# Kernel tuning notes

Measured on AMD Instinct MI355X. Metric: run time of the kernel, lower is better.

Reference implementation:

```python
import jax, jax.numpy as jnp
import numpy as np

N, E, D = 40000, 640000, 128
BN_EPS = 1e-5


def setup_inputs() -> dict:
    key = jax.random.key(0)
    ks = jax.random.split(key, 6)
    x = jax.random.normal(ks[0], (N, D), dtype=jnp.float32)
    src = jax.random.randint(ks[1], (E,), 0, N, dtype=jnp.int64)
    dst = jax.random.randint(ks[2], (E,), 0, N, dtype=jnp.int64)
    W1 = jax.random.normal(ks[3], (D, D), dtype=jnp.float32) * (1.0 / np.sqrt(D))
    b1 = jnp.zeros((D,), dtype=jnp.float32)
    gamma = jnp.ones((D,), dtype=jnp.float32)
    beta = jnp.zeros((D,), dtype=jnp.float32)
    W2 = jax.random.normal(ks[4], (D, D), dtype=jnp.float32) * (1.0 / np.sqrt(D))
    b2 = jnp.zeros((D,), dtype=jnp.float32)
    eps = jnp.zeros((1,), dtype=jnp.float32)
    return {"x": x, "src": src, "dst": dst, "W1": W1, "b1": b1,
            "gamma": gamma, "beta": beta, "W2": W2, "b2": b2, "eps": eps}


def reference(x, src, dst, W1, b1, gamma, beta, W2, b2, eps):
    # edge gather + ReLU + scatter-sum aggregation  (copy_u -> relu -> sum)
    m = jax.nn.relu(x[src])                                  # [E, D]
    agg = jax.ops.segment_sum(m, dst, num_segments=N)        # [N, D]
    h = (1.0 + eps[0]) * x + agg                             # eps-scaled residual
    # MLP: Linear -> BatchNorm1d (batch stats) -> ReLU -> Linear
    h = h @ W1.T + b1
    mu = jnp.mean(h, axis=0)
    var = jnp.var(h, axis=0)                                 # biased, as torch BN
    h = (h - mu) * jax.lax.rsqrt(var + BN_EPS) * gamma + beta
    h = jax.nn.relu(h)
    return h @ W2.T + b2
```

## Files before the change

kernel.cpp:

```cpp
#include <hip/hip_runtime.h>

#define NN 40000
#define NE 640000
#define DD 128
#define CAP 64

typedef __attribute__((ext_vector_type(8))) short short8;
typedef __attribute__((ext_vector_type(4))) float floatx4;

__device__ __forceinline__ unsigned short f2bf(float f) {
    union { float f; unsigned u; } v; v.f = f;
    return (unsigned short)((v.u + 0x7fffu + ((v.u >> 16) & 1u)) >> 16);
}
__device__ __forceinline__ float bflo2f(unsigned u) {
    union { unsigned u; float f; } v; v.u = u << 16; return v.f;
}
__device__ __forceinline__ float bfhi2f(unsigned u) {
    union { unsigned u; float f; } v; v.u = u & 0xffff0000u; return v.f;
}


__global__ void k_convert(const float* __restrict__ x, const float* __restrict__ W1,
                          const float* __restrict__ W2, unsigned short* __restrict__ xb,
                          unsigned short* __restrict__ W1b, unsigned short* __restrict__ W2b) {
    const int tid = blockIdx.x * 256 + threadIdx.x;
    const int P = gridDim.x * 256;
    const float4* x4 = (const float4*)x;
    for (int i = tid; i < NN * DD / 4; i += P) {
        float4 v = x4[i];
        ushort4 o;
        o.x = f2bf(v.x); o.y = f2bf(v.y); o.z = f2bf(v.z); o.w = f2bf(v.w);
        ((ushort4*)xb)[i] = o;
    }
    if (tid < 8192) {
        const float4* w4 = (tid < 4096) ? (const float4*)W1 : (const float4*)W2;
        unsigned short* wb = (tid < 4096) ? W1b : W2b;
        int i = tid & 4095;
        float4 v = w4[i];
        ushort4 o;
        o.x = f2bf(v.x); o.y = f2bf(v.y); o.z = f2bf(v.z); o.w = f2bf(v.w);
        ((ushort4*)wb)[i] = o;
    }
}

__global__ void k_bucket(const int* __restrict__ src, const int* __restrict__ dst,
                         int* __restrict__ cnt, unsigned short* __restrict__ eidx) {
    const int e = blockIdx.x * 256 + threadIdx.x;
    const int d = dst[e];
    const int s = src[e];
    const int slot = atomicAdd(&cnt[d], 1);
    if (slot < CAP) eidx[d * CAP + slot] = (unsigned short)s;
}

__launch_bounds__(256)
__global__ void k_gather(const unsigned short* __restrict__ xb,
                         const unsigned short* __restrict__ eidx,
                         const int* __restrict__ cnt, const float* __restrict__ eps,
                         unsigned short* __restrict__ h) {
    const int n = blockIdx.x * 4 + (threadIdx.x >> 6);
    const int lane = threadIdx.x & 63;
    const unsigned* xw = (const unsigned*)xb;
    const float s = 1.0f + eps[0];
    unsigned xv = xw[n * 64 + lane];
    float ax = bflo2f(xv) * s, ay = bfhi2f(xv) * s;
    int deg = cnt[n];
    deg = (deg > CAP) ? CAP : deg;
    const unsigned short* row = eidx + n * CAP;
    int j = 0;
    for (; j + 3 < deg; j += 4) {
        ushort4 s4 = *(const ushort4*)(row + j);
        unsigned v0 = xw[(int)s4.x * 64 + lane];
        unsigned v1 = xw[(int)s4.y * 64 + lane];
        unsigned v2 = xw[(int)s4.z * 64 + lane];
        unsigned v3 = xw[(int)s4.w * 64 + lane];
        ax += (fmaxf(bflo2f(v0), 0.f) + fmaxf(bflo2f(v1), 0.f)) +
              (fmaxf(bflo2f(v2), 0.f) + fmaxf(bflo2f(v3), 0.f));
        ay += (fmaxf(bfhi2f(v0), 0.f) + fmaxf(bfhi2f(v1), 0.f)) +
              (fmaxf(bfhi2f(v2), 0.f) + fmaxf(bfhi2f(v3), 0.f));
    }
    for (; j < deg; ++j) {
        unsigned v = xw[(int)row[j] * 64 + lane];
        ax += fmaxf(bflo2f(v), 0.f);
        ay += fmaxf(bfhi2f(v), 0.f);
    }
    ((unsigned*)h)[n * 64 + lane] = ((unsigned)f2bf(ay) << 16) | (unsigned)f2bf(ax);
}

__launch_bounds__(256)
__global__ void k_gemm1(const unsigned short* __restrict__ h,
                        const unsigned short* __restrict__ W1b,
                        const float* __restrict__ b1,
                        float* __restrict__ h1, float* __restrict__ stats) {
    __shared__ float red[2][4][DD];
    const int t = threadIdx.x;
    const int wv = t >> 6, lane = t & 63, m = lane & 15, q = lane >> 4;
    const int r0 = blockIdx.x * 64 + wv * 16;
    floatx4 acc[8];
    #pragma unroll
    for (int nt = 0; nt < 8; ++nt) acc[nt] = (floatx4){0.f, 0.f, 0.f, 0.f};
    const unsigned short* arow = h + (r0 + m) * DD + q * 8;
    const unsigned short* brow = W1b + m * DD + q * 8;
    #pragma unroll
    for (int kt = 0; kt < 4; ++kt) {
        short8 a = *(const short8*)(arow + kt * 32);
        #pragma unroll
        for (int nt = 0; nt < 8; ++nt) {
            short8 b = *(const short8*)(brow + nt * 16 * DD + kt * 32);
            acc[nt] = __builtin_amdgcn_mfma_f32_16x16x32_bf16(a, b, acc[nt], 0, 0, 0);
        }
    }
    #pragma unroll
    for (int nt = 0; nt < 8; ++nt) {
        float bv = b1[nt * 16 + m];
        float cs = 0.f, cq = 0.f;
        #pragma unroll
        for (int r = 0; r < 4; ++r) {
            float v = acc[nt][r] + bv;
            h1[(r0 + q * 4 + r) * DD + nt * 16 + m] = v;
            cs += v;
            cq = fmaf(v, v, cq);
        }
        cs += __shfl_xor(cs, 16); cs += __shfl_xor(cs, 32);
        cq += __shfl_xor(cq, 16); cq += __shfl_xor(cq, 32);
        if (q == 0) { red[0][wv][nt * 16 + m] = cs; red[1][wv][nt * 16 + m] = cq; }
    }
    __syncthreads();
    {
        int plane = t >> 7, j = t & 127;
        float v = (red[plane][0][j] + red[plane][1][j]) + (red[plane][2][j] + red[plane][3][j]);
        atomicAdd(stats + plane * DD + j, v);
    }
}

__launch_bounds__(256)
__global__ void k_gemm2(float* __restrict__ io, const unsigned short* __restrict__ W2b,
                        const float* __restrict__ b2, const float* __restrict__ stats,
                        const float* __restrict__ gamma, const float* __restrict__ beta) {
    __shared__ float ssc[DD], ssh[DD];
    const int t = threadIdx.x;
    if (t < DD) {
        const float inv_n = 1.0f / (float)NN;
        float mu = stats[t] * inv_n;
        float var = stats[DD + t] * inv_n - mu * mu;
        float sc = rsqrtf(var + 1e-5f) * gamma[t];
        ssc[t] = sc;
        ssh[t] = beta[t] - mu * sc;
    }
    __syncthreads();
    const int wv = t >> 6, lane = t & 63, m = lane & 15, q = lane >> 4;
    const int r0 = blockIdx.x * 64 + wv * 16;
    floatx4 acc[8];
    #pragma unroll
    for (int nt = 0; nt < 8; ++nt) acc[nt] = (floatx4){0.f, 0.f, 0.f, 0.f};
    const float* arow = io + (r0 + m) * DD + q * 8;
    const unsigned short* brow = W2b + m * DD + q * 8;
    #pragma unroll
    for (int kt = 0; kt < 4; ++kt) {
        const float* ap = arow + kt * 32;
        const int k0 = kt * 32 + q * 8;
        float4 v0 = *(const float4*)(ap);
        float4 v1 = *(const float4*)(ap + 4);
        float4 c0 = *(const float4*)(ssc + k0);
        float4 c1 = *(const float4*)(ssc + k0 + 4);
        float4 d0 = *(const float4*)(ssh + k0);
        float4 d1 = *(const float4*)(ssh + k0 + 4);
        short8 a;
        a[0] = (short)f2bf(fmaxf(fmaf(v0.x, c0.x, d0.x), 0.f));
        a[1] = (short)f2bf(fmaxf(fmaf(v0.y, c0.y, d0.y), 0.f));
        a[2] = (short)f2bf(fmaxf(fmaf(v0.z, c0.z, d0.z), 0.f));
        a[3] = (short)f2bf(fmaxf(fmaf(v0.w, c0.w, d0.w), 0.f));
        a[4] = (short)f2bf(fmaxf(fmaf(v1.x, c1.x, d1.x), 0.f));
        a[5] = (short)f2bf(fmaxf(fmaf(v1.y, c1.y, d1.y), 0.f));
        a[6] = (short)f2bf(fmaxf(fmaf(v1.z, c1.z, d1.z), 0.f));
        a[7] = (short)f2bf(fmaxf(fmaf(v1.w, c1.w, d1.w), 0.f));
        #pragma unroll
        for (int nt = 0; nt < 8; ++nt) {
            short8 b = *(const short8*)(brow + nt * 16 * DD + kt * 32);
            acc[nt] = __builtin_amdgcn_mfma_f32_16x16x32_bf16(a, b, acc[nt], 0, 0, 0);
        }
    }
    #pragma unroll
    for (int nt = 0; nt < 8; ++nt) {
        float bv = b2[nt * 16 + m];
        #pragma unroll
        for (int r = 0; r < 4; ++r)
            io[(r0 + q * 4 + r) * DD + nt * 16 + m] = acc[nt][r] + bv;
    }
}

extern "C" void kernel_launch(void* const* d_in, const int* in_sizes, int n_in,
                              void* d_out, int out_size, void* d_ws, size_t ws_size,
                              hipStream_t stream) {
    const float* x     = (const float*)d_in[0];
    const int*   src   = (const int*)d_in[1];
    const int*   dst   = (const int*)d_in[2];
    const float* W1    = (const float*)d_in[3];
    const float* b1    = (const float*)d_in[4];
    const float* gamma = (const float*)d_in[5];
    const float* beta  = (const float*)d_in[6];
    const float* W2    = (const float*)d_in[7];
    const float* b2    = (const float*)d_in[8];
    const float* eps   = (const float*)d_in[9];
    float* out = (float*)d_out;

    unsigned short* xb  = (unsigned short*)d_ws;
    unsigned short* h   = xb + NN * DD;
    unsigned short* W1b = h + NN * DD;
    unsigned short* W2b = W1b + DD * DD;
    float* stats = (float*)(W2b + DD * DD);
    int*   cnt   = (int*)(stats + 256);
    unsigned short* eidx = (unsigned short*)(cnt + NN);

    hipMemsetAsync(stats, 0, (256 + NN) * sizeof(int), stream);
    hipLaunchKernelGGL(k_convert, dim3(1280),     dim3(256), 0, stream,
                       x, W1, W2, xb, W1b, W2b);
    hipLaunchKernelGGL(k_bucket,  dim3(NE / 256), dim3(256), 0, stream,
                       src, dst, cnt, eidx);
    hipLaunchKernelGGL(k_gather,  dim3(NN / 4),   dim3(256), 0, stream,
                       xb, eidx, cnt, eps, h);
    hipLaunchKernelGGL(k_gemm1,   dim3(NN / 64),  dim3(256), 0, stream,
                       h, W1b, b1, out, stats);
    hipLaunchKernelGGL(k_gemm2,   dim3(NN / 64),  dim3(256), 0, stream,
                       out, W2b, b2, stats, gamma, beta);
}
```

Before: 195.3 us.

## Partition edge bucketing by XCD, widen gather loads, fold memset into convert

```diff
diff --git a/kernel.cpp b/kernel.cpp
--- a/kernel.cpp
+++ b/kernel.cpp
@@ -4,6 +4,7 @@
 #define NE 640000
 #define DD 128
 #define CAP 64
+#define NRANK 312
 
 typedef __attribute__((ext_vector_type(8))) short short8;
 typedef __attribute__((ext_vector_type(4))) float floatx4;
@@ -22,9 +23,11 @@
 
 __global__ void k_convert(const float* __restrict__ x, const float* __restrict__ W1,
                           const float* __restrict__ W2, unsigned short* __restrict__ xb,
-                          unsigned short* __restrict__ W1b, unsigned short* __restrict__ W2b) {
+                          unsigned short* __restrict__ W1b, unsigned short* __restrict__ W2b,
+                          int* __restrict__ zbase) {
     const int tid = blockIdx.x * 256 + threadIdx.x;
     const int P = gridDim.x * 256;
+    for (int i = tid; i < 256 + NN; i += P) zbase[i] = 0;
     const float4* x4 = (const float4*)x;
     for (int i = tid; i < NN * DD / 4; i += P) {
         float4 v = x4[i];
@@ -45,11 +48,18 @@
 
 __global__ void k_bucket(const int* __restrict__ src, const int* __restrict__ dst,
                          int* __restrict__ cnt, unsigned short* __restrict__ eidx) {
-    const int e = blockIdx.x * 256 + threadIdx.x;
-    const int d = dst[e];
-    const int s = src[e];
-    const int slot = atomicAdd(&cnt[d], 1);
-    if (slot < CAP) eidx[d * CAP + slot] = (unsigned short)s;
+    const int xcd = blockIdx.x & 7;
+    const int rank = blockIdx.x >> 3;
+    const int e0 = (int)((long long)rank * NE / NRANK);
+    const int e1 = (int)((long long)(rank + 1) * NE / NRANK);
+    const int lo = xcd * (NN / 8);
+    for (int e = e0 + (int)threadIdx.x; e < e1; e += 256) {
+        int d = dst[e];
+        if ((unsigned)(d - lo) < (unsigned)(NN / 8)) {
+            int slot = atomicAdd(&cnt[d], 1);
+            if (slot < CAP) eidx[d * CAP + slot] = (unsigned short)src[e];
+        }
+    }
 }
 
 __launch_bounds__(256)
@@ -57,33 +67,44 @@
                          const unsigned short* __restrict__ eidx,
                          const int* __restrict__ cnt, const float* __restrict__ eps,
                          unsigned short* __restrict__ h) {
-    const int n = blockIdx.x * 4 + (threadIdx.x >> 6);
-    const int lane = threadIdx.x & 63;
-    const unsigned* xw = (const unsigned*)xb;
+    const int t = threadIdx.x;
+    const int ln = t & 31;
+    const int n = blockIdx.x * 8 + (t >> 5);
+    const uint2* xw = (const uint2*)xb;
     const float s = 1.0f + eps[0];
-    unsigned xv = xw[n * 64 + lane];
-    float ax = bflo2f(xv) * s, ay = bfhi2f(xv) * s;
+    uint2 xv = xw[n * 32 + ln];
+    float a0 = bflo2f(xv.x) * s, a1 = bfhi2f(xv.x) * s;
+    float a2 = bflo2f(xv.y) * s, a3 = bfhi2f(xv.y) * s;
     int deg = cnt[n];
     deg = (deg > CAP) ? CAP : deg;
     const unsigned short* row = eidx + n * CAP;
     int j = 0;
     for (; j + 3 < deg; j += 4) {
         ushort4 s4 = *(const ushort4*)(row + j);
-        unsigned v0 = xw[(int)s4.x * 64 + lane];
-        unsigned v1 = xw[(int)s4.y * 64 + lane];
-        unsigned v2 = xw[(int)s4.z * 64 + lane];
-        unsigned v3 = xw[(int)s4.w * 64 + lane];
-        ax += (fmaxf(bflo2f(v0), 0.f) + fmaxf(bflo2f(v1), 0.f)) +
-              (fmaxf(bflo2f(v2), 0.f) + fmaxf(bflo2f(v3), 0.f));
-        ay += (fmaxf(bfhi2f(v0), 0.f) + fmaxf(bfhi2f(v1), 0.f)) +
-              (fmaxf(bfhi2f(v2), 0.f) + fmaxf(bfhi2f(v3), 0.f));
+        uint2 v0 = xw[(int)s4.x * 32 + ln];
+        uint2 v1 = xw[(int)s4.y * 32 + ln];
+        uint2 v2 = xw[(int)s4.z * 32 + ln];
+        uint2 v3 = xw[(int)s4.w * 32 + ln];
+        a0 += (fmaxf(bflo2f(v0.x), 0.f) + fmaxf(bflo2f(v1.x), 0.f)) +
+              (fmaxf(bflo2f(v2.x), 0.f) + fmaxf(bflo2f(v3.x), 0.f));
+        a1 += (fmaxf(bfhi2f(v0.x), 0.f) + fmaxf(bfhi2f(v1.x), 0.f)) +
+              (fmaxf(bfhi2f(v2.x), 0.f) + fmaxf(bfhi2f(v3.x), 0.f));
+        a2 += (fmaxf(bflo2f(v0.y), 0.f) + fmaxf(bflo2f(v1.y), 0.f)) +
+              (fmaxf(bflo2f(v2.y), 0.f) + fmaxf(bflo2f(v3.y), 0.f));
+        a3 += (fmaxf(bfhi2f(v0.y), 0.f) + fmaxf(bfhi2f(v1.y), 0.f)) +
+              (fmaxf(bfhi2f(v2.y), 0.f) + fmaxf(bfhi2f(v3.y), 0.f));
     }
     for (; j < deg; ++j) {
-        unsigned v = xw[(int)row[j] * 64 + lane];
-        ax += fmaxf(bflo2f(v), 0.f);
-        ay += fmaxf(bfhi2f(v), 0.f);
-    }
-    ((unsigned*)h)[n * 64 + lane] = ((unsigned)f2bf(ay) << 16) | (unsigned)f2bf(ax);
+        uint2 v = xw[(int)row[j] * 32 + ln];
+        a0 += fmaxf(bflo2f(v.x), 0.f);
+        a1 += fmaxf(bfhi2f(v.x), 0.f);
+        a2 += fmaxf(bflo2f(v.y), 0.f);
+        a3 += fmaxf(bfhi2f(v.y), 0.f);
+    }
+    uint2 o;
+    o.x = ((unsigned)f2bf(a1) << 16) | (unsigned)f2bf(a0);
+    o.y = ((unsigned)f2bf(a3) << 16) | (unsigned)f2bf(a2);
+    ((uint2*)h)[n * 32 + ln] = o;
 }
 
 __launch_bounds__(256)
@@ -211,15 +232,14 @@
     int*   cnt   = (int*)(stats + 256);
     unsigned short* eidx = (unsigned short*)(cnt + NN);
 
-    hipMemsetAsync(stats, 0, (256 + NN) * sizeof(int), stream);
-    hipLaunchKernelGGL(k_convert, dim3(1280),     dim3(256), 0, stream,
-                       x, W1, W2, xb, W1b, W2b);
-    hipLaunchKernelGGL(k_bucket,  dim3(NE / 256), dim3(256), 0, stream,
+    hipLaunchKernelGGL(k_convert, dim3(1280),      dim3(256), 0, stream,
+                       x, W1, W2, xb, W1b, W2b, (int*)stats);
+    hipLaunchKernelGGL(k_bucket,  dim3(8 * NRANK), dim3(256), 0, stream,
                        src, dst, cnt, eidx);
-    hipLaunchKernelGGL(k_gather,  dim3(NN / 4),   dim3(256), 0, stream,
+    hipLaunchKernelGGL(k_gather,  dim3(NN / 8),    dim3(256), 0, stream,
                        xb, eidx, cnt, eps, h);
-    hipLaunchKernelGGL(k_gemm1,   dim3(NN / 64),  dim3(256), 0, stream,
+    hipLaunchKernelGGL(k_gemm1,   dim3(NN / 64),   dim3(256), 0, stream,
                        h, W1b, b1, out, stats);
-    hipLaunchKernelGGL(k_gemm2,   dim3(NN / 64),  dim3(256), 0, stream,
+    hipLaunchKernelGGL(k_gemm2,   dim3(NN / 64),   dim3(256), 0, stream,
                        out, W2b, b2, stats, gamma, beta);
 }
```

Result: no change. 193.8 us (-0.8%).
